# Kernel tuning notes

Measured on AMD Instinct MI355X. Metric: run time of the kernel, lower is better.

Reference implementation:

```python
import jax, jax.numpy as jnp
import numpy as np

N_NODES = 50000
N_EDGES = 800000
IN_F = 128
HID = 16
HEADS = 8
OUT_F = 128


def setup_inputs() -> dict:
    key = jax.random.key(0)
    ks = jax.random.split(key, 16)
    h = jax.random.normal(ks[0], (N_NODES, IN_F), dtype=jnp.float32)
    src1 = jax.random.randint(ks[1], (N_EDGES,), 0, N_NODES, dtype=jnp.int32)
    dst1 = jax.random.randint(ks[2], (N_EDGES,), 0, N_NODES, dtype=jnp.int32)
    src2 = jax.random.randint(ks[3], (N_EDGES,), 0, N_NODES, dtype=jnp.int32)
    dst2 = jax.random.randint(ks[4], (N_EDGES,), 0, N_NODES, dtype=jnp.int32)
    norm1 = jax.random.uniform(ks[5], (N_NODES, 1), dtype=jnp.float32)
    norm2 = jax.random.uniform(ks[6], (N_NODES, 1), dtype=jnp.float32)
    D = HEADS * HID  # 128
    W_lin = jax.random.normal(ks[7], (IN_F, D), dtype=jnp.float32) * (1.0 / np.sqrt(IN_F))
    b_lin = jax.random.normal(ks[8], (D,), dtype=jnp.float32) * 0.01
    al = jax.random.normal(ks[9], (HEADS, HID, 1), dtype=jnp.float32) * 0.1
    ar = jax.random.normal(ks[10], (HEADS, HID, 1), dtype=jnp.float32) * 0.1
    W_fc = jax.random.normal(ks[11], (D, OUT_F), dtype=jnp.float32) * (1.0 / np.sqrt(D))
    b_fc = jax.random.normal(ks[12], (OUT_F,), dtype=jnp.float32) * 0.01
    return {"h": h, "src1": src1, "dst1": dst1, "src2": src2, "dst2": dst2,
            "norm1": norm1, "norm2": norm2, "W_lin": W_lin, "b_lin": b_lin,
            "al": al, "ar": ar, "W_fc": W_fc, "b_fc": b_fc}


def _propagate(feat, norm, src, dst, n_nodes):
    # msg = h[src] * norm[src]; accum[v] = sum_{e: dst=v} msg_e; out = accum * norm
    msg = feat[src] * norm[src]                      # [E, D]
    agg = jax.ops.segment_sum(msg, dst, num_segments=n_nodes)
    return agg * norm                                # [N, D]


def _leaky_relu(x):
    return jnp.where(x > 0, x, 0.2 * x)


def reference(h, src1, dst1, src2, dst2, norm1, norm2, W_lin, b_lin, al, ar, W_fc, b_fc):
    N = h.shape[0]
    hf = h @ W_lin + b_lin                           # [N, 8*HID] (dropout p given but eval-mode -> identity)
    h1 = _propagate(hf, norm1, src1, dst1, N)
    h2 = _propagate(hf, norm2, src2, dst2, N)
    # Faithful to torch: row-major reshape [N, 8*HID] -> (8, N, HID)
    h1r = h1.reshape(HEADS, N, HID)
    h2r = h2.reshape(HEADS, N, HID)
    hr = hf.reshape(HEADS, N, HID)
    ai = jnp.einsum('hnd,hdo->hno', hr, al)          # [8, N, 1]
    aj1 = jnp.einsum('hnd,hdo->hno', h1r, ar)
    aj2 = jnp.einsum('hnd,hdo->hno', h2r, ar)
    a1 = jnp.clip(jnp.exp(_leaky_relu(ai + aj1)), -10.0, 10.0)
    a2 = jnp.clip(jnp.exp(_leaky_relu(ai + aj2)), -10.0, 10.0)
    denom = a1 + a2
    out = (a1 / denom) * h1r + (a2 / denom) * h2r    # [8, N, HID]
    out = out.reshape(N, HEADS * HID)
    return out @ W_fc + b_fc
```

## Files before the change

### kernel.cpp

```cpp
#include <hip/hip_runtime.h>

#define NN 50000
#define NE 800000
#define NB 196
#define NBG 392
#define NBLK 128
#define CHUNK 6250
#define MAXB 6144

typedef __bf16 bf16x8 __attribute__((ext_vector_type(8)));
typedef float  f32x4  __attribute__((ext_vector_type(4)));

__device__ __forceinline__ unsigned short f2bf(float x) {
    unsigned u = __float_as_uint(x);
    return (unsigned short)((u + 0x7FFFu + ((u >> 16) & 1u)) >> 16);
}
__device__ __forceinline__ float bflo(unsigned u) { return __uint_as_float(u << 16); }
__device__ __forceinline__ float bfhi(unsigned u) { return __uint_as_float(u & 0xFFFF0000u); }
__device__ __forceinline__ unsigned pack2(float a, float b) {
    return (unsigned)f2bf(a) | ((unsigned)f2bf(b) << 16);
}

__global__ __launch_bounds__(1024) void histA_kernel(
    const int* __restrict__ dst1, const int* __restrict__ dst2, int* __restrict__ histG,
    const float* __restrict__ Wa, const float* __restrict__ Wb,
    unsigned short* __restrict__ Wta, unsigned short* __restrict__ Wtb)
{
    const int t = threadIdx.x, blk = blockIdx.x;
    if (blk >= NBLK) {
        const float* W = (blk - NBLK) ? Wb : Wa;
        unsigned short* Wt = (blk - NBLK) ? Wtb : Wta;
        for (int j = t; j < 128 * 128; j += 1024) {
            int n = j >> 7, k = j & 127;
            Wt[j] = f2bf(W[k * 128 + n]);
        }
        return;
    }
    __shared__ int h[NBG];
    for (int i = t; i < NBG; i += 1024) h[i] = 0;
    __syncthreads();
    const int base = blk * CHUNK;
    for (int i = t; i < CHUNK; i += 1024) {
        atomicAdd(&h[dst1[base + i] >> 8], 1);
        atomicAdd(&h[NB + (dst2[base + i] >> 8)], 1);
    }
    __syncthreads();
    for (int i = t; i < NBG; i += 1024)
        histG[blk * NBG + i] = h[i];
}

__global__ __launch_bounds__(1024) void scatterC_kernel(
    const int* __restrict__ src1, const int* __restrict__ dst1,
    const int* __restrict__ src2, const int* __restrict__ dst2,
    const int* __restrict__ histG,
    int* __restrict__ gbbase, int* __restrict__ gbtot,
    unsigned int* __restrict__ bin1, unsigned int* __restrict__ bin2)
{
    __shared__ int s[512];
    __shared__ int pos[NBG];
    const int t = threadIdx.x, blk = blockIdx.x;

    int total_i = 0, pref_i = 0;
    if (t < NBG) {
        for (int c = 0; c < NBLK; c++) {
            int v = histG[c * NBG + t];
            total_i += v;
            if (c < blk) pref_i += v;
        }
    }
    if (t < 512) s[t] = (t < NBG) ? total_i : 0;
    __syncthreads();
    for (int off = 1; off < 512; off <<= 1) {
        int x = 0;
        if (t < 512 && t >= off) x = s[t - off];
        __syncthreads();
        if (t < 512) s[t] += x;
        __syncthreads();
    }
    const int sumG1 = s[NB - 1];
    if (t < NBG) {
        int excl = s[t] - total_i;
        int bb = excl - ((t >= NB) ? sumG1 : 0);
        pos[t] = bb + pref_i;
        if (blk == 0) { gbbase[t] = bb; gbtot[t] = total_i; }
    }
    __syncthreads();

    const int base = blk * CHUNK;
    for (int i = t; i < CHUNK; i += 1024) {
        int d = dst1[base + i], sv = src1[base + i];
        int slot = atomicAdd(&pos[d >> 8], 1);
        bin1[slot] = ((unsigned)(d & 255) << 16) | (unsigned)sv;
        d = dst2[base + i]; sv = src2[base + i];
        slot = atomicAdd(&pos[NB + (d >> 8)], 1);
        bin2[slot] = ((unsigned)(d & 255) << 16) | (unsigned)sv;
    }
}

__global__ __launch_bounds__(256) void bucket_sort_kernel(
    const unsigned int* __restrict__ bin1, const unsigned int* __restrict__ bin2,
    const int* __restrict__ bbase, const int* __restrict__ btot,
    unsigned short* __restrict__ csr1, int* __restrict__ start1, int* __restrict__ deg1,
    unsigned short* __restrict__ csr2, int* __restrict__ start2, int* __restrict__ deg2)
{
    __shared__ int lcnt[256];
    __shared__ int sc[256];
    __shared__ int oat[256];
    __shared__ unsigned short outb[MAXB];
    const int t = threadIdx.x;
    const int g = (blockIdx.x >= NB) ? 1 : 0;
    const int b = blockIdx.x - g * NB;
    const unsigned int* bin = g ? bin2 : bin1;
    unsigned short* csr = g ? csr2 : csr1;
    int* start = g ? start2 : start1;
    int* deg   = g ? deg2 : deg1;

    const int base = bbase[g * NB + b];
    const int tot = min(btot[g * NB + b], MAXB);

    lcnt[t] = 0;
    __syncthreads();
    for (int i = t; i < tot; i += 256) atomicAdd(&lcnt[bin[base + i] >> 16], 1);
    __syncthreads();
    sc[t] = lcnt[t];
    __syncthreads();
    for (int off = 1; off < 256; off <<= 1) {
        int x = (t >= off) ? sc[t - off] : 0;
        __syncthreads();
        sc[t] += x;
        __syncthreads();
    }
    const int ex = sc[t] - lcnt[t];
    oat[t] = ex;
    __syncthreads();
    for (int i = t; i < tot; i += 256) {
        unsigned v = bin[base + i];
        int slot = atomicAdd(&oat[v >> 16], 1);
        outb[slot] = (unsigned short)(v & 0xFFFFu);
    }
    __syncthreads();
    for (int i = t; i < tot; i += 256) csr[base + i] = outb[i];
    int nd = b * 256 + t;
    if (nd < NN) { start[nd] = base + ex; deg[nd] = lcnt[t]; }
}

__global__ __launch_bounds__(256) void mfma_gemm_kernel(
    const float* __restrict__ X, const unsigned short* __restrict__ Wt,
    const float* __restrict__ bias, unsigned short* __restrict__ Ybf, int nrows)
{
    __shared__ unsigned short Wl[128 * 128];
    const int t = threadIdx.x;
    const int lane = t & 63;
    const int wv = t >> 6;
    const int row0 = blockIdx.x * 64;
    const int m16 = lane & 15;
    const int quad = lane >> 4;

    {
        const uint4* Wg = (const uint4*)Wt;
        #pragma unroll
        for (int i = 0; i < 8; i++) {
            int gi = t + i * 256;
            int n = gi >> 4, g = gi & 15;
            uint4 v = Wg[gi];
            *(uint4*)&Wl[n * 128 + (((g ^ (n & 15)) << 3))] = v;
        }
    }

    const int arow = row0 + wv * 16 + m16;
    const bool valid = (arow < nrows);
    const float4* X4 = (const float4*)X;
    float4 xr[8];
    #pragma unroll
    for (int kc = 0; kc < 4; kc++) {
        if (valid) {
            int gidx = arow * 32 + kc * 8 + quad * 2;
            xr[kc * 2]     = X4[gidx];
            xr[kc * 2 + 1] = X4[gidx + 1];
        } else {
            xr[kc * 2] = xr[kc * 2 + 1] = make_float4(0.f, 0.f, 0.f, 0.f);
        }
    }
    __syncthreads();

    f32x4 acc[8];
    #pragma unroll
    for (int nt = 0; nt < 8; nt++) acc[nt] = (f32x4){0.f, 0.f, 0.f, 0.f};

    #pragma unroll
    for (int kc = 0; kc < 4; kc++) {
        union { unsigned short u[8]; bf16x8 v; } ah, al;
        float f[8] = { xr[kc*2].x, xr[kc*2].y, xr[kc*2].z, xr[kc*2].w,
                       xr[kc*2+1].x, xr[kc*2+1].y, xr[kc*2+1].z, xr[kc*2+1].w };
        #pragma unroll
        for (int j = 0; j < 8; j++) {
            unsigned u = __float_as_uint(f[j]);
            ah.u[j] = (unsigned short)(u >> 16);
            al.u[j] = f2bf(f[j] - __uint_as_float(u & 0xFFFF0000u));
        }
        const int sgbase = (kc * 4 + quad);
        #pragma unroll
        for (int nt = 0; nt < 8; nt++) {
            const int n = nt * 16 + m16;
            bf16x8 b = *(const bf16x8*)&Wl[n * 128 + ((sgbase ^ m16) << 3)];
            acc[nt] = __builtin_amdgcn_mfma_f32_16x16x32_bf16(ah.v, b, acc[nt], 0, 0, 0);
            acc[nt] = __builtin_amdgcn_mfma_f32_16x16x32_bf16(al.v, b, acc[nt], 0, 0, 0);
        }
    }

    #pragma unroll
    for (int nt = 0; nt < 8; nt++) {
        const int col = nt * 16 + m16;
        const float bc = bias[col];
        #pragma unroll
        for (int r = 0; r < 4; r++) {
            int row = row0 + wv * 16 + quad * 4 + r;
            if (row < nrows) Ybf[(long)row * 128 + col] = f2bf(acc[nt][r] + bc);
        }
    }
}

__global__ __launch_bounds__(256) void mfma_gemm_bf16_kernel(
    const unsigned short* __restrict__ Xbf, const unsigned short* __restrict__ Wt,
    const float* __restrict__ bias, float* __restrict__ Y, int nrows)
{
    __shared__ unsigned short Wl[128 * 128];
    const int t = threadIdx.x;
    const int lane = t & 63;
    const int wv = t >> 6;
    const int row0 = blockIdx.x * 64;
    const int m16 = lane & 15;
    const int quad = lane >> 4;

    {
        const uint4* Wg = (const uint4*)Wt;
        #pragma unroll
        for (int i = 0; i < 8; i++) {
            int gi = t + i * 256;
            int n = gi >> 4, g = gi & 15;
            uint4 v = Wg[gi];
            *(uint4*)&Wl[n * 128 + (((g ^ (n & 15)) << 3))] = v;
        }
    }

    const int arow = row0 + wv * 16 + m16;
    const bool valid = (arow < nrows);
    const uint4* X16 = (const uint4*)Xbf;
    union { uint4 u; bf16x8 v; } xr[4];
    #pragma unroll
    for (int kc = 0; kc < 4; kc++) {
        if (valid) xr[kc].u = X16[arow * 16 + kc * 4 + quad];
        else       xr[kc].u = make_uint4(0, 0, 0, 0);
    }
    __syncthreads();

    f32x4 acc[8];
    #pragma unroll
    for (int nt = 0; nt < 8; nt++) acc[nt] = (f32x4){0.f, 0.f, 0.f, 0.f};

    #pragma unroll
    for (int kc = 0; kc < 4; kc++) {
        const int sgbase = (kc * 4 + quad);
        #pragma unroll
        for (int nt = 0; nt < 8; nt++) {
            const int n = nt * 16 + m16;
            bf16x8 b = *(const bf16x8*)&Wl[n * 128 + ((sgbase ^ m16) << 3)];
            acc[nt] = __builtin_amdgcn_mfma_f32_16x16x32_bf16(xr[kc].v, b, acc[nt], 0, 0, 0);
        }
    }

    #pragma unroll
    for (int nt = 0; nt < 8; nt++) {
        const int col = nt * 16 + m16;
        const float bc = bias[col];
        #pragma unroll
        for (int r = 0; r < 4; r++) {
            int row = row0 + wv * 16 + quad * 4 + r;
            if (row < nrows) Y[(long)row * 128 + col] = acc[nt][r] + bc;
        }
    }
}

#define GA_LOAD(dst, ndst, myc, nv, E, NB_) {                              \
    int e_ = (E); int ec_ = (e_ < (NB_)) ? e_ : 0;                         \
    int sx_ = __shfl((myc), ec_);                                          \
    float nq_ = __shfl((nv), ec_);                                         \
    ndst = (e_ < (NB_)) ? nq_ : 0.f;                                       \
    dst = *(const uint4*)(tblb + (((long)sx_) << 8) + sub16); }

#define GA_ISSUE8(p, myc, nv, J0, NB_)                                     \
    GA_LOAD(p##0, n##p##0, myc, nv, (J0) + 0  + qtr, NB_)                  \
    GA_LOAD(p##1, n##p##1, myc, nv, (J0) + 4  + qtr, NB_)                  \
    GA_LOAD(p##2, n##p##2, myc, nv, (J0) + 8  + qtr, NB_)                  \
    GA_LOAD(p##3, n##p##3, myc, nv, (J0) + 12 + qtr, NB_)                  \
    GA_LOAD(p##4, n##p##4, myc, nv, (J0) + 16 + qtr, NB_)                  \
    GA_LOAD(p##5, n##p##5, myc, nv, (J0) + 20 + qtr, NB_)                  \
    GA_LOAD(p##6, n##p##6, myc, nv, (J0) + 24 + qtr, NB_)                  \
    GA_LOAD(p##7, n##p##7, myc, nv, (J0) + 28 + qtr, NB_)

#define GA_CONS1(v, n, c)                                                  \
    c##0 = fmaf(bflo(v.x), n, c##0); c##1 = fmaf(bfhi(v.x), n, c##1);      \
    c##2 = fmaf(bflo(v.y), n, c##2); c##3 = fmaf(bfhi(v.y), n, c##3);      \
    c##4 = fmaf(bflo(v.z), n, c##4); c##5 = fmaf(bfhi(v.z), n, c##5);      \
    c##6 = fmaf(bflo(v.w), n, c##6); c##7 = fmaf(bfhi(v.w), n, c##7);

#define GA_CONS8(p, c)                                                     \
    GA_CONS1(p##0, n##p##0, c) GA_CONS1(p##1, n##p##1, c)                  \
    GA_CONS1(p##2, n##p##2, c) GA_CONS1(p##3, n##p##3, c)                  \
    GA_CONS1(p##4, n##p##4, c) GA_CONS1(p##5, n##p##5, c)                  \
    GA_CONS1(p##6, n##p##6, c) GA_CONS1(p##7, n##p##7, c)

__global__ __launch_bounds__(256, 4) void gather_attn_kernel(
    const unsigned short* __restrict__ hfb,
    const unsigned short* __restrict__ csr1, const int* __restrict__ start1,
    const int* __restrict__ deg1, const float* __restrict__ norm1,
    const unsigned short* __restrict__ csr2, const int* __restrict__ start2,
    const int* __restrict__ deg2, const float* __restrict__ norm2,
    const float* __restrict__ al, const float* __restrict__ ar,
    unsigned short* __restrict__ outb)
{
    const int lane = threadIdx.x & 63;
    const int wv = threadIdx.x >> 6;
    int node = blockIdx.x * 4 + wv;
    node = __builtin_amdgcn_readfirstlane(node);
    const char* tblb = (const char*)hfb;
    const int qtr = lane >> 4;
    const int sub16 = (lane & 15) * 16;

    const uint4 ufv = *(const uint4*)(tblb + ((long)node << 8) + sub16);

    const int st1 = start1[node], dg1 = deg1[node];
    const int st2 = start2[node], dg2 = deg2[node];
    const int dgc1 = (dg1 < 64) ? dg1 : 64;
    const int dgc2 = (dg2 < 64) ? dg2 : 64;

    int myc1 = (lane < dgc1) ? (int)csr1[st1 + lane] : 0;
    int myc2 = (lane < dgc2) ? (int)csr2[st2 + lane] : 0;
    const float nv1 = norm1[myc1];
    const float nv2 = norm2[myc2];

    float c10=0.f,c11=0.f,c12=0.f,c13=0.f,c14=0.f,c15=0.f,c16=0.f,c17=0.f;
    float c20=0.f,c21=0.f,c22=0.f,c23=0.f,c24=0.f,c25=0.f,c26=0.f,c27=0.f;

    uint4 a0,a1,a2,a3,a4,a5,a6,a7, b0,b1,b2,b3,b4,b5,b6,b7;
    float na0,na1,na2,na3,na4,na5,na6,na7, nb0,nb1,nb2,nb3,nb4,nb5,nb6,nb7;

    GA_ISSUE8(a, myc1, nv1, 0, dgc1)
    GA_ISSUE8(b, myc2, nv2, 0, dgc2)
    __builtin_amdgcn_sched_barrier(0);
    GA_CONS8(a, c1)
    GA_CONS8(b, c2)

    if (dgc1 > 32) {
        GA_ISSUE8(a, myc1, nv1, 32, dgc1)
        __builtin_amdgcn_sched_barrier(0);
        GA_CONS8(a, c1)
    }
    if (dgc2 > 32) {
        GA_ISSUE8(b, myc2, nv2, 32, dgc2)
        __builtin_amdgcn_sched_barrier(0);
        GA_CONS8(b, c2)
    }

    for (int base = 64; base < dg1; base += 64) {
        const int nbv = ((dg1 - base) < 64) ? (dg1 - base) : 64;
        int myc = (lane < nbv) ? (int)csr1[st1 + base + lane] : 0;
        const float nv = norm1[myc];
        GA_ISSUE8(a, myc, nv, 0, nbv)
        __builtin_amdgcn_sched_barrier(0);
        GA_CONS8(a, c1)
        if (nbv > 32) {
            GA_ISSUE8(a, myc, nv, 32, nbv)
            __builtin_amdgcn_sched_barrier(0);
            GA_CONS8(a, c1)
        }
    }
    for (int base = 64; base < dg2; base += 64) {
        const int nbv = ((dg2 - base) < 64) ? (dg2 - base) : 64;
        int myc = (lane < nbv) ? (int)csr2[st2 + base + lane] : 0;
        const float nv = norm2[myc];
        GA_ISSUE8(b, myc, nv, 0, nbv)
        __builtin_amdgcn_sched_barrier(0);
        GA_CONS8(b, c2)
        if (nbv > 32) {
            GA_ISSUE8(b, myc, nv, 32, nbv)
            __builtin_amdgcn_sched_barrier(0);
            GA_CONS8(b, c2)
        }
    }

    float acc1[8] = {c10,c11,c12,c13,c14,c15,c16,c17};
    float acc2[8] = {c20,c21,c22,c23,c24,c25,c26,c27};

    #pragma unroll
    for (int i = 0; i < 8; i++) {
        acc1[i] += __shfl_xor(acc1[i], 16);
        acc1[i] += __shfl_xor(acc1[i], 32);
        acc2[i] += __shfl_xor(acc2[i], 16);
        acc2[i] += __shfl_xor(acc2[i], 32);
    }

    const float nn1 = norm1[node], nn2 = norm2[node];

    const int m = lane & 15;
    const int head = (node * 8 + (m >> 1)) / NN;
    const int hb = head * 16 + ((m & 1) << 3);
    float uff[8] = { bflo(ufv.x), bfhi(ufv.x), bflo(ufv.y), bfhi(ufv.y),
                     bflo(ufv.z), bfhi(ufv.z), bflo(ufv.w), bfhi(ufv.w) };
    float s_ai = 0.f, s1 = 0.f, s2 = 0.f;
    #pragma unroll
    for (int i = 0; i < 8; i++) {
        acc1[i] *= nn1;
        acc2[i] *= nn2;
        const float avi = al[hb + i], rvi = ar[hb + i];
        s_ai = fmaf(uff[i], avi, s_ai);
        s1   = fmaf(acc1[i], rvi, s1);
        s2   = fmaf(acc2[i], rvi, s2);
    }
    s_ai += __shfl_xor(s_ai, 1);
    s1   += __shfl_xor(s1, 1);
    s2   += __shfl_xor(s2, 1);

    float x1 = s_ai + s1; x1 = x1 > 0.f ? x1 : 0.2f * x1;
    float x2 = s_ai + s2; x2 = x2 > 0.f ? x2 : 0.2f * x2;
    float e1 = fminf(expf(x1), 10.f);
    float e2 = fminf(expf(x2), 10.f);
    float inv = 1.f / (e1 + e2);
    float w1 = e1 * inv, w2 = e2 * inv;

    if (lane < 16) {
        uint4 w;
        w.x = pack2(w1 * acc1[0] + w2 * acc2[0], w1 * acc1[1] + w2 * acc2[1]);
        w.y = pack2(w1 * acc1[2] + w2 * acc2[2], w1 * acc1[3] + w2 * acc2[3]);
        w.z = pack2(w1 * acc1[4] + w2 * acc2[4], w1 * acc1[5] + w2 * acc2[5]);
        w.w = pack2(w1 * acc1[6] + w2 * acc2[6], w1 * acc1[7] + w2 * acc2[7]);
        *(uint4*)((char*)outb + ((long)node << 8) + m * 16) = w;
    }
}

extern "C" void kernel_launch(void* const* d_in, const int* in_sizes, int n_in,
                              void* d_out, int out_size, void* d_ws, size_t ws_size,
                              hipStream_t stream)
{
    const float* h     = (const float*)d_in[0];
    const int*   src1  = (const int*)  d_in[1];
    const int*   dst1  = (const int*)  d_in[2];
    const int*   src2  = (const int*)  d_in[3];
    const int*   dst2  = (const int*)  d_in[4];
    const float* norm1 = (const float*)d_in[5];
    const float* norm2 = (const float*)d_in[6];
    const float* W_lin = (const float*)d_in[7];
    const float* b_lin = (const float*)d_in[8];
    const float* al    = (const float*)d_in[9];
    const float* ar    = (const float*)d_in[10];
    const float* W_fc  = (const float*)d_in[11];
    const float* b_fc  = (const float*)d_in[12];
    float* out = (float*)d_out;

    unsigned short* hfb  = (unsigned short*)d_ws;
    unsigned short* outbf = hfb + (size_t)NN * 128;
    unsigned int* bin1 = (unsigned int*)(outbf + (size_t)NN * 128);
    unsigned int* bin2 = bin1 + NE;
    unsigned short* csr1 = (unsigned short*)(bin2 + NE);
    unsigned short* csr2 = csr1 + NE;
    unsigned short* WtL  = csr2 + NE;
    unsigned short* WtF  = WtL + 128 * 128;
    int* histG  = (int*)(WtF + 128 * 128);
    int* btot   = histG + NBLK * NBG;
    int* bbase  = btot + NBG;
    int* start1 = bbase + NBG;
    int* start2 = start1 + NN;
    int* deg1   = start2 + NN;
    int* deg2   = deg1 + NN;

    histA_kernel<<<NBLK + 2, 1024, 0, stream>>>(dst1, dst2, histG, W_lin, W_fc, WtL, WtF);

    mfma_gemm_kernel<<<(NN + 63) / 64, 256, 0, stream>>>(h, WtL, b_lin, hfb, NN);

    scatterC_kernel<<<NBLK, 1024, 0, stream>>>(src1, dst1, src2, dst2, histG,
                                               bbase, btot, bin1, bin2);

    bucket_sort_kernel<<<NBG, 256, 0, stream>>>(bin1, bin2, bbase, btot,
                                                csr1, start1, deg1,
                                                csr2, start2, deg2);

    gather_attn_kernel<<<12500, 256, 0, stream>>>(
        hfb,
        csr1, start1, deg1, norm1,
        csr2, start2, deg2, norm2,
        al, ar, outbf);

    mfma_gemm_bf16_kernel<<<(NN + 63) / 64, 256, 0, stream>>>(outbf, WtF, b_fc, out, NN);
}
```

Measured before the change: 269.2 us.

## Split node feature table into two column halves for cache-friendly gather

The first GEMM now writes its bf16 output as two separate 64-column tables, and the gather kernel launches twice as many blocks, each handling one half of the features for its nodes. Block indices are interleaved so that groups of blocks working on the same half run close together, which shrinks the working set of the random gathers to better fit in cache. Each wavefront now processes 8 neighbors per pass with 8 lanes per row and falls back to a serial per-edge loop for degrees above 32. That loop risks slowdowns on high-degree nodes, and the CSR, norm and degree reads are now duplicated across the two halves.

```diff
diff --git a/kernel.cpp b/kernel.cpp
--- a/kernel.cpp
+++ b/kernel.cpp
@@ -146,7 +146,8 @@
 
 __global__ __launch_bounds__(256) void mfma_gemm_kernel(
     const float* __restrict__ X, const unsigned short* __restrict__ Wt,
-    const float* __restrict__ bias, unsigned short* __restrict__ Ybf, int nrows)
+    const float* __restrict__ bias,
+    unsigned short* __restrict__ YA, unsigned short* __restrict__ YB, int nrows)
 {
     __shared__ unsigned short Wl[128 * 128];
     const int t = threadIdx.x;
@@ -215,7 +216,11 @@
         #pragma unroll
         for (int r = 0; r < 4; r++) {
             int row = row0 + wv * 16 + quad * 4 + r;
-            if (row < nrows) Ybf[(long)row * 128 + col] = f2bf(acc[nt][r] + bc);
+            if (row < nrows) {
+                float val = acc[nt][r] + bc;
+                if (col < 64) YA[(long)row * 64 + col]        = f2bf(val);
+                else          YB[(long)row * 64 + (col - 64)] = f2bf(val);
+            }
         }
     }
 }
@@ -286,17 +291,13 @@
     int sx_ = __shfl((myc), ec_);                                          \
     float nq_ = __shfl((nv), ec_);                                         \
     ndst = (e_ < (NB_)) ? nq_ : 0.f;                                       \
-    dst = *(const uint4*)(tblb + (((long)sx_) << 8) + sub16); }
-
-#define GA_ISSUE8(p, myc, nv, J0, NB_)                                     \
-    GA_LOAD(p##0, n##p##0, myc, nv, (J0) + 0  + qtr, NB_)                  \
-    GA_LOAD(p##1, n##p##1, myc, nv, (J0) + 4  + qtr, NB_)                  \
-    GA_LOAD(p##2, n##p##2, myc, nv, (J0) + 8  + qtr, NB_)                  \
-    GA_LOAD(p##3, n##p##3, myc, nv, (J0) + 12 + qtr, NB_)                  \
-    GA_LOAD(p##4, n##p##4, myc, nv, (J0) + 16 + qtr, NB_)                  \
-    GA_LOAD(p##5, n##p##5, myc, nv, (J0) + 20 + qtr, NB_)                  \
-    GA_LOAD(p##6, n##p##6, myc, nv, (J0) + 24 + qtr, NB_)                  \
-    GA_LOAD(p##7, n##p##7, myc, nv, (J0) + 28 + qtr, NB_)
+    dst = *(const uint4*)(tblb + (((long)sx_) << 7) + sub16); }
+
+#define GA_ISSUE4(p, myc, nv, NB_)                                         \
+    GA_LOAD(p##0, n##p##0, myc, nv, 0  + grp, NB_)                         \
+    GA_LOAD(p##1, n##p##1, myc, nv, 8  + grp, NB_)                         \
+    GA_LOAD(p##2, n##p##2, myc, nv, 16 + grp, NB_)                         \
+    GA_LOAD(p##3, n##p##3, myc, nv, 24 + grp, NB_)
 
 #define GA_CONS1(v, n, c)                                                  \
     c##0 = fmaf(bflo(v.x), n, c##0); c##1 = fmaf(bfhi(v.x), n, c##1);      \
@@ -304,14 +305,12 @@
     c##4 = fmaf(bflo(v.z), n, c##4); c##5 = fmaf(bfhi(v.z), n, c##5);      \
     c##6 = fmaf(bflo(v.w), n, c##6); c##7 = fmaf(bfhi(v.w), n, c##7);
 
-#define GA_CONS8(p, c)                                                     \
+#define GA_CONS4(p, c)                                                     \
     GA_CONS1(p##0, n##p##0, c) GA_CONS1(p##1, n##p##1, c)                  \
-    GA_CONS1(p##2, n##p##2, c) GA_CONS1(p##3, n##p##3, c)                  \
-    GA_CONS1(p##4, n##p##4, c) GA_CONS1(p##5, n##p##5, c)                  \
-    GA_CONS1(p##6, n##p##6, c) GA_CONS1(p##7, n##p##7, c)
-
-__global__ __launch_bounds__(256, 4) void gather_attn_kernel(
-    const unsigned short* __restrict__ hfb,
+    GA_CONS1(p##2, n##p##2, c) GA_CONS1(p##3, n##p##3, c)
+
+__global__ __launch_bounds__(256) void gather_attn_kernel(
+    const unsigned short* __restrict__ hfA, const unsigned short* __restrict__ hfB,
     const unsigned short* __restrict__ csr1, const int* __restrict__ start1,
     const int* __restrict__ deg1, const float* __restrict__ norm1,
     const unsigned short* __restrict__ csr2, const int* __restrict__ start2,
@@ -321,18 +320,19 @@
 {
     const int lane = threadIdx.x & 63;
     const int wv = threadIdx.x >> 6;
-    int node = blockIdx.x * 4 + wv;
+    const int b = blockIdx.x;
+    const int half = (b >> 2) & 1;
+    const int lb = (b >> 3) * 4 + (b & 3);
+    int node = lb * 4 + wv;
     node = __builtin_amdgcn_readfirstlane(node);
-    const char* tblb = (const char*)hfb;
-    const int qtr = lane >> 4;
-    const int sub16 = (lane & 15) * 16;
-
-    const uint4 ufv = *(const uint4*)(tblb + ((long)node << 8) + sub16);
+    const char* tblb = (const char*)(half ? hfB : hfA);
+    const int grp = lane >> 3;
+    const int sub16 = (lane & 7) * 16;
 
     const int st1 = start1[node], dg1 = deg1[node];
     const int st2 = start2[node], dg2 = deg2[node];
-    const int dgc1 = (dg1 < 64) ? dg1 : 64;
-    const int dgc2 = (dg2 < 64) ? dg2 : 64;
+    const int dgc1 = (dg1 < 32) ? dg1 : 32;
+    const int dgc2 = (dg2 < 32) ? dg2 : 32;
 
     int myc1 = (lane < dgc1) ? (int)csr1[st1 + lane] : 0;
     int myc2 = (lane < dgc2) ? (int)csr2[st2 + lane] : 0;
@@ -341,70 +341,53 @@
 
     float c10=0.f,c11=0.f,c12=0.f,c13=0.f,c14=0.f,c15=0.f,c16=0.f,c17=0.f;
     float c20=0.f,c21=0.f,c22=0.f,c23=0.f,c24=0.f,c25=0.f,c26=0.f,c27=0.f;
-
-    uint4 a0,a1,a2,a3,a4,a5,a6,a7, b0,b1,b2,b3,b4,b5,b6,b7;
-    float na0,na1,na2,na3,na4,na5,na6,na7, nb0,nb1,nb2,nb3,nb4,nb5,nb6,nb7;
-
-    GA_ISSUE8(a, myc1, nv1, 0, dgc1)
-    GA_ISSUE8(b, myc2, nv2, 0, dgc2)
+    uint4 a0, a1, a2, a3, b0, b1, b2, b3;
+    float na0, na1, na2, na3, nb0, nb1, nb2, nb3;
+
+    GA_ISSUE4(a, myc1, nv1, dgc1)
+    GA_ISSUE4(b, myc2, nv2, dgc2)
+    const uint4 ufv = *(const uint4*)(tblb + ((long)node << 7) + sub16);
     __builtin_amdgcn_sched_barrier(0);
-    GA_CONS8(a, c1)
-    GA_CONS8(b, c2)
-
-    if (dgc1 > 32) {
-        GA_ISSUE8(a, myc1, nv1, 32, dgc1)
-        __builtin_amdgcn_sched_barrier(0);
-        GA_CONS8(a, c1)
-    }
-    if (dgc2 > 32) {
-        GA_ISSUE8(b, myc2, nv2, 32, dgc2)
-        __builtin_amdgcn_sched_barrier(0);
-        GA_CONS8(b, c2)
-    }
-
-    for (int base = 64; base < dg1; base += 64) {
-        const int nbv = ((dg1 - base) < 64) ? (dg1 - base) : 64;
-        int myc = (lane < nbv) ? (int)csr1[st1 + base + lane] : 0;
-        const float nv = norm1[myc];
-        GA_ISSUE8(a, myc, nv, 0, nbv)
-        __builtin_amdgcn_sched_barrier(0);
-        GA_CONS8(a, c1)
-        if (nbv > 32) {
-            GA_ISSUE8(a, myc, nv, 32, nbv)
-            __builtin_amdgcn_sched_barrier(0);
-            GA_CONS8(a, c1)
-        }
-    }
-    for (int base = 64; base < dg2; base += 64) {
-        const int nbv = ((dg2 - base) < 64) ? (dg2 - base) : 64;
-        int myc = (lane < nbv) ? (int)csr2[st2 + base + lane] : 0;
-        const float nv = norm2[myc];
-        GA_ISSUE8(b, myc, nv, 0, nbv)
-        __builtin_amdgcn_sched_barrier(0);
-        GA_CONS8(b, c2)
-        if (nbv > 32) {
-            GA_ISSUE8(b, myc, nv, 32, nbv)
-            __builtin_amdgcn_sched_barrier(0);
-            GA_CONS8(b, c2)
-        }
-    }
+    GA_CONS4(a, c1)
+    GA_CONS4(b, c2)
 
     float acc1[8] = {c10,c11,c12,c13,c14,c15,c16,c17};
     float acc2[8] = {c20,c21,c22,c23,c24,c25,c26,c27};
-
     #pragma unroll
     for (int i = 0; i < 8; i++) {
+        acc1[i] += __shfl_xor(acc1[i], 8);
         acc1[i] += __shfl_xor(acc1[i], 16);
         acc1[i] += __shfl_xor(acc1[i], 32);
+        acc2[i] += __shfl_xor(acc2[i], 8);
         acc2[i] += __shfl_xor(acc2[i], 16);
         acc2[i] += __shfl_xor(acc2[i], 32);
     }
 
+    for (int e = 32; e < dg1; e++) {
+        int s = (int)csr1[st1 + e];
+        float n = norm1[s];
+        uint4 v = *(const uint4*)(tblb + ((long)s << 7) + sub16);
+        acc1[0] = fmaf(bflo(v.x), n, acc1[0]); acc1[1] = fmaf(bfhi(v.x), n, acc1[1]);
+        acc1[2] = fmaf(bflo(v.y), n, acc1[2]); acc1[3] = fmaf(bfhi(v.y), n, acc1[3]);
+        acc1[4] = fmaf(bflo(v.z), n, acc1[4]); acc1[5] = fmaf(bfhi(v.z), n, acc1[5]);
+        acc1[6] = fmaf(bflo(v.w), n, acc1[6]); acc1[7] = fmaf(bfhi(v.w), n, acc1[7]);
+    }
+    for (int e = 32; e < dg2; e++) {
+        int s = (int)csr2[st2 + e];
+        float n = norm2[s];
+        uint4 v = *(const uint4*)(tblb + ((long)s << 7) + sub16);
+        acc2[0] = fmaf(bflo(v.x), n, acc2[0]); acc2[1] = fmaf(bfhi(v.x), n, acc2[1]);
+        acc2[2] = fmaf(bflo(v.y), n, acc2[2]); acc2[3] = fmaf(bfhi(v.y), n, acc2[3]);
+        acc2[4] = fmaf(bflo(v.z), n, acc2[4]); acc2[5] = fmaf(bfhi(v.z), n, acc2[5]);
+        acc2[6] = fmaf(bflo(v.w), n, acc2[6]); acc2[7] = fmaf(bfhi(v.w), n, acc2[7]);
+    }
+
     const float nn1 = norm1[node], nn2 = norm2[node];
 
-    const int m = lane & 15;
-    const int head = (node * 8 + (m >> 1)) / NN;
-    const int hb = head * 16 + ((m & 1) << 3);
+    const int mm = lane & 7;
+    const int cc = half * 4 + (mm >> 1);
+    const int head = (node * 8 + cc) / NN;
+    const int hb = head * 16 + ((mm & 1) << 3);
     float uff[8] = { bflo(ufv.x), bfhi(ufv.x), bflo(ufv.y), bfhi(ufv.y),
                      bflo(ufv.z), bfhi(ufv.z), bflo(ufv.w), bfhi(ufv.w) };
     float s_ai = 0.f, s1 = 0.f, s2 = 0.f;
@@ -428,13 +411,13 @@
     float inv = 1.f / (e1 + e2);
     float w1 = e1 * inv, w2 = e2 * inv;
 
-    if (lane < 16) {
+    if (lane < 8) {
         uint4 w;
         w.x = pack2(w1 * acc1[0] + w2 * acc2[0], w1 * acc1[1] + w2 * acc2[1]);
         w.y = pack2(w1 * acc1[2] + w2 * acc2[2], w1 * acc1[3] + w2 * acc2[3]);
         w.z = pack2(w1 * acc1[4] + w2 * acc2[4], w1 * acc1[5] + w2 * acc2[5]);
         w.w = pack2(w1 * acc1[6] + w2 * acc2[6], w1 * acc1[7] + w2 * acc2[7]);
-        *(uint4*)((char*)outb + ((long)node << 8) + m * 16) = w;
+        *(uint4*)((char*)outb + ((long)node << 8) + half * 128 + mm * 16) = w;
     }
 }
 
@@ -457,8 +440,9 @@
     const float* b_fc  = (const float*)d_in[12];
     float* out = (float*)d_out;
 
-    unsigned short* hfb  = (unsigned short*)d_ws;
-    unsigned short* outbf = hfb + (size_t)NN * 128;
+    unsigned short* hfA  = (unsigned short*)d_ws;
+    unsigned short* hfB  = hfA + (size_t)NN * 64;
+    unsigned short* outbf = hfB + (size_t)NN * 64;
     unsigned int* bin1 = (unsigned int*)(outbf + (size_t)NN * 128);
     unsigned int* bin2 = bin1 + NE;
     unsigned short* csr1 = (unsigned short*)(bin2 + NE);
@@ -475,7 +459,7 @@
 
     histA_kernel<<<NBLK + 2, 1024, 0, stream>>>(dst1, dst2, histG, W_lin, W_fc, WtL, WtF);
 
-    mfma_gemm_kernel<<<(NN + 63) / 64, 256, 0, stream>>>(h, WtL, b_lin, hfb, NN);
+    mfma_gemm_kernel<<<(NN + 63) / 64, 256, 0, stream>>>(h, WtL, b_lin, hfA, hfB, NN);
 
     scatterC_kernel<<<NBLK, 1024, 0, stream>>>(src1, dst1, src2, dst2, histG,
                                                bbase, btot, bin1, bin2);
@@ -484,8 +468,8 @@
                                                 csr1, start1, deg1,
                                                 csr2, start2, deg2);
 
-    gather_attn_kernel<<<12500, 256, 0, stream>>>(
-        hfb,
+    gather_attn_kernel<<<25000, 256, 0, stream>>>(
+        hfA, hfB,
         csr1, start1, deg1, norm1,
         csr2, start2, deg2, norm2,
         al, ar, outbf);
```

Result: faster. 249.8 us (-7.2%).
